# Performance work log

Measured on AMD Instinct MI355X. Metric: run time of the kernel, lower is better.

Reference implementation:

```python
import jax, jax.numpy as jnp
import numpy as np

DIM = 512
HEADS = 16
HD = DIM // HEADS            # head_dim = 32
WH, WW = 8, 8                # window_size
D0, D1 = 2, 2                # dilated_size
TWH, TWW = WH * D0, WW * D1  # total_window_size = 16,16
SCALE = HD ** -0.5


def _wpart(x, wh, ww):
    # (B,H,W,C) -> (B * H/wh * W/ww, wh, ww, C)
    B, H, W, C = x.shape
    x = x.reshape(B, H // wh, wh, W // ww, ww, C)
    return x.transpose(0, 1, 3, 2, 4, 5).reshape(-1, wh, ww, C)


def _wrev(win, wh, ww, H, W):
    # (nW*B, wh, ww, C) -> (B, H, W, C)
    C = win.shape[-1]
    B = win.shape[0] // ((H // wh) * (W // ww))
    x = win.reshape(B, H // wh, W // ww, wh, ww, C).transpose(0, 1, 3, 2, 4, 5)
    return x.reshape(B, H, W, C)


def _rope2(x):
    # 2D RoPE over a (B, WH, WW, HD) window: first half of HD rotated by row
    # position, second half by column position (axial rotary embedding).
    d = HD // 2
    inv = 1.0 / (10000.0 ** (jnp.arange(0, d, 2, dtype=jnp.float32) / d))  # (d/2,)

    def rot(xp, ang):
        x1, x2 = xp[..., 0::2], xp[..., 1::2]
        c, s = jnp.cos(ang), jnp.sin(ang)
        return jnp.stack([x1 * c - x2 * s, x1 * s + x2 * c], axis=-1).reshape(xp.shape)

    ah = (jnp.arange(WH, dtype=jnp.float32)[:, None] * inv)[:, None, :]  # (WH,1,d/2)
    aw = (jnp.arange(WW, dtype=jnp.float32)[:, None] * inv)[None, :, :]  # (1,WW,d/2)
    return jnp.concatenate([rot(x[..., :d], ah), rot(x[..., d:], aw)], axis=-1)


def _forward(x, qkv_w, qkv_b, proj_w, proj_b):
    B, H, W, C = x.shape
    # partition into total windows, then dilated regrouping
    xw = _wpart(x, TWH, TWW)                                   # (B_, 16, 16, C)
    B_ = xw.shape[0]
    xw = _wpart(xw, D0, D1)                                    # (B_*64, 2, 2, C)
    xw = xw.reshape(B_, WH * WW, D0 * D1, C)
    xw = xw.transpose(0, 2, 1, 3).reshape(B_ * D0 * D1, WH * WW, C)  # (B__, N, C)
    B__, N = xw.shape[0], xw.shape[1]

    qkv = (xw @ qkv_w.T + qkv_b).reshape(B__, N, 3, HEADS, HD).transpose(2, 0, 3, 1, 4)
    q, k, v = qkv[0], qkv[1], qkv[2]                           # (B__, HEADS, N, HD)

    q = _rope2(q.reshape(-1, WH, WW, HD)).reshape(B__, HEADS, N, HD) * SCALE
    k = _rope2(k.reshape(-1, WH, WW, HD)).reshape(B__, HEADS, N, HD)

    attn = jax.nn.softmax(jnp.einsum('bhnd,bhmd->bhnm', q, k), axis=-1)
    out = jnp.einsum('bhnm,bhmd->bhnd', attn, v)               # (B__, HEADS, N, HD)
    out = out.transpose(0, 2, 1, 3).reshape(B__, N, C)

    # undo dilated regrouping, then undo total-window partition
    out = out.reshape(B_, D0 * D1, N, C).transpose(0, 2, 1, 3).reshape(-1, D0, D1, C)
    out = _wrev(out, D0, D1, TWH, TWW)                         # (B_, 16, 16, C)
    out = _wrev(out, TWH, TWW, H, W)                           # (B, H, W, C)
    return out @ proj_w.T + proj_b


def setup_inputs() -> dict:
    key = jax.random.key(0)
    k0, k1, k2 = jax.random.split(key, 3)
    x = jax.random.normal(k0, (4, 128, 128, DIM), dtype=jnp.float32)
    qkv_w = jax.random.normal(k1, (3 * DIM, DIM), dtype=jnp.float32) * (DIM ** -0.5)
    qkv_b = jnp.zeros((3 * DIM,), dtype=jnp.float32)
    proj_w = jax.random.normal(k2, (DIM, DIM), dtype=jnp.float32) * (DIM ** -0.5)
    proj_b = jnp.zeros((DIM,), dtype=jnp.float32)
    return {"x": x, "qkv_w": qkv_w, "qkv_b": qkv_b, "proj_w": proj_w, "proj_b": proj_b}


def reference(x, qkv_w, qkv_b, proj_w, proj_b):
    return _forward(x, qkv_w, qkv_b, proj_w, proj_b)
```

## Files before the change

### kernel.cpp

```cpp
#include <hip/hip_runtime.h>
#include <hip/hip_bf16.h>
#include <stdint.h>

#define DIMC  512
#define NHEAD 16
#define HDIM  32
#define NTOK  65536
#define QKVN  1536
static constexpr float SCALE_F = 0.17677669529663687f;

typedef __attribute__((ext_vector_type(4))) float  f32x4;
typedef __attribute__((ext_vector_type(8))) __bf16 bf16x8;

__device__ __forceinline__ uint16_t f2bf(float f) {
  union { float f; uint32_t u; } v; v.f = f;
  return (uint16_t)((v.u + 0x7FFFu + ((v.u >> 16) & 1u)) >> 16);
}

__device__ __forceinline__ void gload_lds16(const void* g, void* l) {
  __builtin_amdgcn_global_load_lds((const __attribute__((address_space(1))) void*)g,
                                   (__attribute__((address_space(3))) void*)l,
                                   16, 0, 0);
}

__global__ void cvt_f32_bf16(const float* __restrict__ src,
                             uint16_t* __restrict__ dst, int n4)
{
  int i = blockIdx.x * blockDim.x + threadIdx.x;
  const int stride = gridDim.x * blockDim.x;
  for (; i < n4; i += stride) {
    const float4 v = ((const float4*)src)[i];
    ushort4 o;
    o.x = f2bf(v.x); o.y = f2bf(v.y); o.z = f2bf(v.z); o.w = f2bf(v.w);
    ((ushort4*)dst)[i] = o;
  }
}

template <bool OUT_F32>
__global__ __launch_bounds__(256, 2)
void gemm_bias_bf16(const uint16_t* __restrict__ A,
                    const uint16_t* __restrict__ B,
                    const float* __restrict__ bias,
                    void* __restrict__ Cv,
                    int M, int N, int K)
{
  __shared__ __align__(16) __bf16 As[128][64];
  __shared__ __align__(16) __bf16 Bs[128][64];

  const int tid = threadIdx.x;
  const int l  = tid & 63, w = tid >> 6;
  const int wm = w >> 1,  wn = w & 1;
  const int lm = l & 15,  lq = l >> 4;
  const long m0 = (long)blockIdx.y * 128;
  const long n0 = (long)blockIdx.x * 128;

  const int srow = tid >> 3;
  const int scol = (tid & 7) * 8;
  const uint16_t* Ag = A + (m0 + srow) * (long)K + scol;
  const uint16_t* Bg = B + (n0 + srow) * (long)K + scol;
  char* AsW = (char*)(&As[0][0]) + w * 1024;
  char* BsW = (char*)(&Bs[0][0]) + w * 1024;

  f32x4 acc[4][4] = {};

  for (int kt = 0; kt < K; kt += 64) {
#pragma unroll
    for (int c = 0; c < 4; ++c)
      gload_lds16(Ag + (size_t)c * 32 * K + kt, AsW + c * 4096);
#pragma unroll
    for (int c = 0; c < 4; ++c)
      gload_lds16(Bg + (size_t)c * 32 * K + kt, BsW + c * 4096);
    __syncthreads();

#pragma unroll
    for (int kk = 0; kk < 2; ++kk) {
      bf16x8 a[4], b[4];
#pragma unroll
      for (int i = 0; i < 4; ++i)
        a[i] = *(const bf16x8*)(&As[wm * 64 + i * 16 + lm][kk * 32 + lq * 8]);
#pragma unroll
      for (int i = 0; i < 4; ++i)
        b[i] = *(const bf16x8*)(&Bs[wn * 64 + i * 16 + lm][kk * 32 + lq * 8]);
#pragma unroll
      for (int mi = 0; mi < 4; ++mi)
#pragma unroll
        for (int ni = 0; ni < 4; ++ni)
          acc[mi][ni] = __builtin_amdgcn_mfma_f32_16x16x32_bf16(
              a[mi], b[ni], acc[mi][ni], 0, 0, 0);
    }
    __syncthreads();
  }

  float bvals[4];
#pragma unroll
  for (int ni = 0; ni < 4; ++ni)
    bvals[ni] = bias[n0 + wn * 64 + ni * 16 + lm];

#pragma unroll
  for (int mi = 0; mi < 4; ++mi)
#pragma unroll
    for (int ni = 0; ni < 4; ++ni) {
      long m = m0 + wm * 64 + mi * 16 + lq * 4;
      long n = n0 + wn * 64 + ni * 16 + lm;
#pragma unroll
      for (int r = 0; r < 4; ++r) {
        const float val = acc[mi][ni][r] + bvals[ni];
        if (OUT_F32) ((float*)Cv)[(m + r) * (long)N + n] = val;
        else         ((uint16_t*)Cv)[(m + r) * (long)N + n] = f2bf(val);
      }
    }
}

__global__ void attn_win(const uint16_t* __restrict__ QKV,
                         uint16_t* __restrict__ O)
{
  __shared__ __align__(16) __bf16 Pl[4][64][72];

  const int tid = threadIdx.x;
  const int l  = tid & 63, w = tid >> 6;
  const int lm = l & 15,  lq = l >> 4;
  const int bid = blockIdx.x;
  const int g = bid >> 2;
  const int h = (bid & 3) * 4 + w;

  const int d1 = g & 1, d0 = (g >> 1) & 1;
  const int wx = (g >> 2) & 7, wy = (g >> 5) & 7, bb = g >> 8;
  const long tbase = ((long)(bb * 128 + wy * 16 + d0) * 128) + wx * 16 + d1;

  f32x4 invs;
#pragma unroll
  for (int i = 0; i < 4; ++i)
    invs[i] = exp2f(-1.6609640474436813f * (float)((lq & 1) * 4 + i));

  const int co_q = h * HDIM;
  const int co_k = DIMC + h * HDIM;
  const int co_v = 2 * DIMC + h * HDIM;

  bf16x8 qf[4], kf[4];
#pragma unroll
  for (int f = 0; f < 4; ++f) {
    const int n  = f * 16 + lm;
    const int iy = n >> 3, ix = n & 7;
    const float pos = (lq < 2) ? (float)iy : (float)ix;
    const long t = tbase + iy * 256 + ix * 2;
    const uint16_t* qp = QKV + t * QKVN + co_q + lq * 8;
    const uint16_t* kp = QKV + t * QKVN + co_k + lq * 8;
    {
      bf16x8 raw = *(const bf16x8*)qp, o;
#pragma unroll
      for (int i = 0; i < 4; ++i) {
        float x1 = (float)raw[2 * i], x2 = (float)raw[2 * i + 1];
        float s, c; __sincosf(pos * invs[i], &s, &c);
        o[2 * i]     = (__bf16)((x1 * c - x2 * s) * SCALE_F);
        o[2 * i + 1] = (__bf16)((x1 * s + x2 * c) * SCALE_F);
      }
      qf[f] = o;
    }
    {
      bf16x8 raw = *(const bf16x8*)kp, o;
#pragma unroll
      for (int i = 0; i < 4; ++i) {
        float x1 = (float)raw[2 * i], x2 = (float)raw[2 * i + 1];
        float s, c; __sincosf(pos * invs[i], &s, &c);
        o[2 * i]     = (__bf16)(x1 * c - x2 * s);
        o[2 * i + 1] = (__bf16)(x1 * s + x2 * c);
      }
      kf[f] = o;
    }
  }

  const f32x4 fzero = {0.f, 0.f, 0.f, 0.f};
  f32x4 s[4][4];
#pragma unroll
  for (int mi = 0; mi < 4; ++mi)
#pragma unroll
    for (int ni = 0; ni < 4; ++ni)
      s[mi][ni] = __builtin_amdgcn_mfma_f32_16x16x32_bf16(qf[mi], kf[ni], fzero, 0, 0, 0);

  float rsum[4][4];
#pragma unroll
  for (int mi = 0; mi < 4; ++mi)
#pragma unroll
    for (int r = 0; r < 4; ++r) {
      float m = s[mi][0][r];
#pragma unroll
      for (int ni = 1; ni < 4; ++ni) m = fmaxf(m, s[mi][ni][r]);
      m = fmaxf(m, __shfl_xor(m, 1));
      m = fmaxf(m, __shfl_xor(m, 2));
      m = fmaxf(m, __shfl_xor(m, 4));
      m = fmaxf(m, __shfl_xor(m, 8));
      float sum = 0.f;
#pragma unroll
      for (int ni = 0; ni < 4; ++ni) {
        float p = expf(s[mi][ni][r] - m);
        s[mi][ni][r] = p;
        sum += p;
      }
      sum += __shfl_xor(sum, 1);
      sum += __shfl_xor(sum, 2);
      sum += __shfl_xor(sum, 4);
      sum += __shfl_xor(sum, 8);
      rsum[mi][r] = sum;
    }

#pragma unroll
  for (int mi = 0; mi < 4; ++mi)
#pragma unroll
    for (int ni = 0; ni < 4; ++ni)
#pragma unroll
      for (int r = 0; r < 4; ++r)
        Pl[w][mi * 16 + lq * 4 + r][ni * 16 + lm] = (__bf16)s[mi][ni][r];

  bf16x8 pa[4][2];
#pragma unroll
  for (int mi = 0; mi < 4; ++mi)
#pragma unroll
    for (int kk = 0; kk < 2; ++kk)
      pa[mi][kk] = *(const bf16x8*)(&Pl[w][mi * 16 + lm][kk * 32 + lq * 8]);

  bf16x8 vf[2][2];
#pragma unroll
  for (int kk = 0; kk < 2; ++kk)
#pragma unroll
    for (int n2 = 0; n2 < 2; ++n2) {
      const int nb = kk * 32 + lq * 8;
      const long tb2 = tbase + (long)(nb >> 3) * 256;
      const uint16_t* vp = QKV + co_v + n2 * 16 + lm;
      bf16x8 o;
#pragma unroll
      for (int i = 0; i < 8; ++i)
        o[i] = *(const __bf16*)(vp + (tb2 + 2 * i) * QKVN);
      vf[kk][n2] = o;
    }

  f32x4 oacc[4][2] = {};
#pragma unroll
  for (int kk = 0; kk < 2; ++kk)
#pragma unroll
    for (int mi = 0; mi < 4; ++mi)
#pragma unroll
      for (int n2 = 0; n2 < 2; ++n2)
        oacc[mi][n2] = __builtin_amdgcn_mfma_f32_16x16x32_bf16(
            pa[mi][kk], vf[kk][n2], oacc[mi][n2], 0, 0, 0);

#pragma unroll
  for (int mi = 0; mi < 4; ++mi)
#pragma unroll
    for (int r = 0; r < 4; ++r) {
      const int n = mi * 16 + lq * 4 + r;
      const long t = tbase + (n >> 3) * 256 + (n & 7) * 2;
      const float rinv = 1.0f / rsum[mi][r];
#pragma unroll
      for (int n2 = 0; n2 < 2; ++n2)
        O[t * DIMC + h * HDIM + n2 * 16 + lm] = f2bf(oacc[mi][n2][r] * rinv);
    }
}

extern "C" void kernel_launch(void* const* d_in, const int* in_sizes, int n_in,
                              void* d_out, int out_size, void* d_ws, size_t ws_size,
                              hipStream_t stream)
{
  const float* x      = (const float*)d_in[0];
  const float* qkv_w  = (const float*)d_in[1];
  const float* qkv_b  = (const float*)d_in[2];
  const float* proj_w = (const float*)d_in[3];
  const float* proj_b = (const float*)d_in[4];
  float* out = (float*)d_out;

  uint16_t* xb    = (uint16_t*)d_ws;
  uint16_t* qwb   = xb    + (size_t)NTOK * DIMC;
  uint16_t* pwb   = qwb   + (size_t)QKVN * DIMC;
  uint16_t* qkv   = pwb   + (size_t)DIMC * DIMC;
  uint16_t* attn  = qkv   + (size_t)NTOK * QKVN;

  cvt_f32_bf16<<<2048, 256, 0, stream>>>(x,      xb,  NTOK * DIMC / 4);
  cvt_f32_bf16<<<512,  256, 0, stream>>>(qkv_w,  qwb, QKVN * DIMC / 4);
  cvt_f32_bf16<<<256,  256, 0, stream>>>(proj_w, pwb, DIMC * DIMC / 4);

  gemm_bias_bf16<false><<<dim3(QKVN / 128, NTOK / 128), dim3(256), 0, stream>>>(
      xb, qwb, qkv_b, qkv, NTOK, QKVN, DIMC);

  attn_win<<<dim3(1024 * 4), dim3(256), 0, stream>>>(qkv, attn);

  gemm_bias_bf16<true><<<dim3(DIMC / 128, NTOK / 128), dim3(256), 0, stream>>>(
      attn, pwb, proj_b, out, NTOK, DIMC, DIMC);
}
```

Before: 317.6 us.

## Replace GEMM with 256x256 tiled, double-buffered 8-phase pipelined kernel

```diff
diff --git a/kernel.cpp b/kernel.cpp
--- a/kernel.cpp
+++ b/kernel.cpp
@@ -37,78 +37,117 @@
 }
 
 template <bool OUT_F32>
-__global__ __launch_bounds__(256, 2)
-void gemm_bias_bf16(const uint16_t* __restrict__ A,
-                    const uint16_t* __restrict__ B,
-                    const float* __restrict__ bias,
-                    void* __restrict__ Cv,
-                    int M, int N, int K)
+__global__ __launch_bounds__(512, 2)
+void gemm256_8ph(const uint16_t* __restrict__ A,
+                 const uint16_t* __restrict__ B,
+                 const float* __restrict__ bias,
+                 void* __restrict__ Cv,
+                 int M, int N, int K, int gx)
 {
-  __shared__ __align__(16) __bf16 As[128][64];
-  __shared__ __align__(16) __bf16 Bs[128][64];
+  __shared__ __align__(16) char lds[131072];
 
   const int tid = threadIdx.x;
   const int l  = tid & 63, w = tid >> 6;
-  const int wm = w >> 1,  wn = w & 1;
+  const int wm = w >> 2,  wn = w & 3;
   const int lm = l & 15,  lq = l >> 4;
-  const long m0 = (long)blockIdx.y * 128;
-  const long n0 = (long)blockIdx.x * 128;
-
-  const int srow = tid >> 3;
-  const int scol = (tid & 7) * 8;
-  const uint16_t* Ag = A + (m0 + srow) * (long)K + scol;
-  const uint16_t* Bg = B + (n0 + srow) * (long)K + scol;
-  char* AsW = (char*)(&As[0][0]) + w * 1024;
-  char* BsW = (char*)(&Bs[0][0]) + w * 1024;
-
-  f32x4 acc[4][4] = {};
-
-  for (int kt = 0; kt < K; kt += 64) {
-#pragma unroll
-    for (int c = 0; c < 4; ++c)
-      gload_lds16(Ag + (size_t)c * 32 * K + kt, AsW + c * 4096);
-#pragma unroll
-    for (int c = 0; c < 4; ++c)
-      gload_lds16(Bg + (size_t)c * 32 * K + kt, BsW + c * 4096);
-    __syncthreads();
-
-#pragma unroll
-    for (int kk = 0; kk < 2; ++kk) {
-      bf16x8 a[4], b[4];
-#pragma unroll
-      for (int i = 0; i < 4; ++i)
-        a[i] = *(const bf16x8*)(&As[wm * 64 + i * 16 + lm][kk * 32 + lq * 8]);
-#pragma unroll
-      for (int i = 0; i < 4; ++i)
-        b[i] = *(const bf16x8*)(&Bs[wn * 64 + i * 16 + lm][kk * 32 + lq * 8]);
-#pragma unroll
-      for (int mi = 0; mi < 4; ++mi)
-#pragma unroll
-        for (int ni = 0; ni < 4; ++ni)
-          acc[mi][ni] = __builtin_amdgcn_mfma_f32_16x16x32_bf16(
-              a[mi], b[ni], acc[mi][ni], 0, 0, 0);
-    }
-    __syncthreads();
-  }
-
-  float bvals[4];
-#pragma unroll
-  for (int ni = 0; ni < 4; ++ni)
-    bvals[ni] = bias[n0 + wn * 64 + ni * 16 + lm];
-
-#pragma unroll
-  for (int mi = 0; mi < 4; ++mi)
-#pragma unroll
-    for (int ni = 0; ni < 4; ++ni) {
-      long m = m0 + wm * 64 + mi * 16 + lq * 4;
-      long n = n0 + wn * 64 + ni * 16 + lm;
-#pragma unroll
-      for (int r = 0; r < 4; ++r) {
-        const float val = acc[mi][ni][r] + bvals[ni];
-        if (OUT_F32) ((float*)Cv)[(m + r) * (long)N + n] = val;
-        else         ((uint16_t*)Cv)[(m + r) * (long)N + n] = f2bf(val);
-      }
-    }
+
+  const int nwg = gridDim.x;
+  const int qq = nwg >> 3, rr = nwg & 7;
+  const int xcd = blockIdx.x & 7, loc = blockIdx.x >> 3;
+  const int sw = (xcd < rr ? xcd * (qq + 1) : rr * (qq + 1) + (xcd - rr) * qq) + loc;
+  const long m0 = (long)(sw / gx) * 256;
+  const long n0 = (long)(sw % gx) * 256;
+
+  const int srow  = tid >> 3;
+  const int scolb = (((tid & 7) ^ (srow & 7)) << 4);
+  const uint16_t* Ags = A + (m0 + srow) * (long)K + (scolb >> 1);
+  const uint16_t* Bgs = B + (n0 + srow) * (long)K + (scolb >> 1);
+  char* ldsW = lds + (w << 10);
+
+  auto STAGE = [&](const uint16_t* Gs, int regionOff, int half, int kt) {
+    const uint16_t* s0 = Gs + (size_t)(half * 128) * K + kt;
+    gload_lds16(s0,                 ldsW + regionOff);
+    gload_lds16(s0 + (size_t)64 * K, ldsW + regionOff + 8192);
+  };
+
+  const int colx0 = ((lq ^ (lm & 7)) << 4);
+  const int aoff0 = (wm * 64 + lm) * 128 + colx0;
+  const int aoff1 = (wm * 64 + lm) * 128 + (colx0 ^ 64);
+  const int boff0 = (wn * 32 + lm) * 128 + colx0;
+  const int boff1 = (wn * 32 + lm) * 128 + (colx0 ^ 64);
+
+  f32x4 acc[2][2][4][2] = {};
+
+#define PHASE(SLOT, QM, QN, STG, VM)                                          \
+  {                                                                           \
+    const char* Ab = lds + (SLOT) * 65536 + (QM) * 16384;                     \
+    const char* Bb = lds + (SLOT) * 65536 + 32768 + (QN) * 16384;             \
+    bf16x8 af0[4], af1[4], bq0[2], bq1[2];                                    \
+    _Pragma("unroll") for (int i = 0; i < 4; ++i) {                           \
+      af0[i] = *(const bf16x8*)(Ab + aoff0 + i * 2048);                       \
+      af1[i] = *(const bf16x8*)(Ab + aoff1 + i * 2048);                       \
+    }                                                                         \
+    _Pragma("unroll") for (int j = 0; j < 2; ++j) {                           \
+      bq0[j] = *(const bf16x8*)(Bb + boff0 + j * 2048);                       \
+      bq1[j] = *(const bf16x8*)(Bb + boff1 + j * 2048);                       \
+    }                                                                         \
+    STG;                                                                      \
+    __builtin_amdgcn_s_barrier();                                             \
+    __builtin_amdgcn_s_setprio(1);                                            \
+    _Pragma("unroll") for (int i = 0; i < 4; ++i)                             \
+      _Pragma("unroll") for (int j = 0; j < 2; ++j) {                         \
+        acc[QM][QN][i][j] = __builtin_amdgcn_mfma_f32_16x16x32_bf16(          \
+            af0[i], bq0[j], acc[QM][QN][i][j], 0, 0, 0);                      \
+        acc[QM][QN][i][j] = __builtin_amdgcn_mfma_f32_16x16x32_bf16(          \
+            af1[i], bq1[j], acc[QM][QN][i][j], 0, 0, 0);                      \
+      }                                                                       \
+    __builtin_amdgcn_s_setprio(0);                                            \
+    if (VM) { asm volatile("s_waitcnt vmcnt(4)" ::: "memory"); }              \
+    __builtin_amdgcn_s_barrier();                                             \
+  }
+
+  STAGE(Ags, 0,             0, 0);
+  STAGE(Bgs, 32768,         0, 0);
+  STAGE(Ags, 16384,         1, 0);
+  STAGE(Bgs, 49152,         1, 0);
+  STAGE(Ags, 65536,         0, 64);
+  STAGE(Bgs, 65536 + 32768, 0, 64);
+  asm volatile("s_waitcnt vmcnt(4)" ::: "memory");
+  __builtin_amdgcn_s_barrier();
+
+  for (int t2 = 0; t2 < K / 64; t2 += 2) {
+    const int k1 = (t2 + 1) * 64;
+    int k2 = (t2 + 2) * 64; if (k2 >= K) k2 = 0;
+    int k3 = (t2 + 3) * 64; if (k3 >= K) k3 = 0;
+    PHASE(0, 0, 0, STAGE(Ags, 65536 + 16384, 1, k1), 0)
+    PHASE(0, 0, 1, STAGE(Bgs, 65536 + 49152, 1, k1), 0)
+    PHASE(0, 1, 0, STAGE(Ags, 0,             0, k2), 0)
+    PHASE(0, 1, 1, STAGE(Bgs, 32768,         0, k2), 1)
+    PHASE(1, 0, 0, STAGE(Ags, 16384,         1, k2), 0)
+    PHASE(1, 0, 1, STAGE(Bgs, 49152,         1, k2), 0)
+    PHASE(1, 1, 0, STAGE(Ags, 65536,         0, k3), 0)
+    PHASE(1, 1, 1, STAGE(Bgs, 65536 + 32768, 0, k3), 1)
+  }
+#undef PHASE
+
+#pragma unroll
+  for (int qm = 0; qm < 2; ++qm)
+#pragma unroll
+  for (int qn = 0; qn < 2; ++qn)
+#pragma unroll
+  for (int i = 0; i < 4; ++i)
+#pragma unroll
+  for (int j = 0; j < 2; ++j) {
+    const long m = m0 + qm * 128 + wm * 64 + i * 16 + lq * 4;
+    const long n = n0 + qn * 128 + wn * 32 + j * 16 + lm;
+    const float bv = bias[n];
+#pragma unroll
+    for (int r = 0; r < 4; ++r) {
+      const float val = acc[qm][qn][i][j][r] + bv;
+      if (OUT_F32) ((float*)Cv)[(m + r) * (long)N + n] = val;
+      else         ((uint16_t*)Cv)[(m + r) * (long)N + n] = f2bf(val);
+    }
+  }
 }
 
 __global__ void attn_win(const uint16_t* __restrict__ QKV,
@@ -277,11 +316,11 @@
   cvt_f32_bf16<<<512,  256, 0, stream>>>(qkv_w,  qwb, QKVN * DIMC / 4);
   cvt_f32_bf16<<<256,  256, 0, stream>>>(proj_w, pwb, DIMC * DIMC / 4);
 
-  gemm_bias_bf16<false><<<dim3(QKVN / 128, NTOK / 128), dim3(256), 0, stream>>>(
-      xb, qwb, qkv_b, qkv, NTOK, QKVN, DIMC);
+  gemm256_8ph<false><<<dim3((NTOK / 256) * (QKVN / 256)), dim3(512), 0, stream>>>(
+      xb, qwb, qkv_b, qkv, NTOK, QKVN, DIMC, QKVN / 256);
 
   attn_win<<<dim3(1024 * 4), dim3(256), 0, stream>>>(qkv, attn);
 
-  gemm_bias_bf16<true><<<dim3(DIMC / 128, NTOK / 128), dim3(256), 0, stream>>>(
-      attn, pwb, proj_b, out, NTOK, DIMC, DIMC);
-}
+  gemm256_8ph<true><<<dim3((NTOK / 256) * (DIMC / 256)), dim3(512), 0, stream>>>(
+      attn, pwb, proj_b, out, NTOK, DIMC, DIMC, DIMC / 256);
+}
```

New measurement: 304.2 us. 4.2% less time.

## Fuse x fp32-to-bf16 conversion into QKV GEMM with swizzled LDS and XCD remap

Applied to the files above, without the earlier changes.

```diff
diff --git a/kernel.cpp b/kernel.cpp
--- a/kernel.cpp
+++ b/kernel.cpp
@@ -36,13 +36,13 @@
   }
 }
 
-template <bool OUT_F32>
-__global__ __launch_bounds__(256, 2)
-void gemm_bias_bf16(const uint16_t* __restrict__ A,
-                    const uint16_t* __restrict__ B,
-                    const float* __restrict__ bias,
-                    void* __restrict__ Cv,
-                    int M, int N, int K)
+template <bool A_F32, bool OUT_F32>
+__global__ __launch_bounds__(256, 3)
+void gemm128_tlp(const void* __restrict__ Av,
+                 const uint16_t* __restrict__ B,
+                 const float* __restrict__ bias,
+                 void* __restrict__ Cv,
+                 int M, int N, int K, int gx)
 {
   __shared__ __align__(16) __bf16 As[128][64];
   __shared__ __align__(16) __bf16 Bs[128][64];
@@ -51,36 +51,86 @@
   const int l  = tid & 63, w = tid >> 6;
   const int wm = w >> 1,  wn = w & 1;
   const int lm = l & 15,  lq = l >> 4;
-  const long m0 = (long)blockIdx.y * 128;
-  const long n0 = (long)blockIdx.x * 128;
-
-  const int srow = tid >> 3;
-  const int scol = (tid & 7) * 8;
-  const uint16_t* Ag = A + (m0 + srow) * (long)K + scol;
-  const uint16_t* Bg = B + (n0 + srow) * (long)K + scol;
-  char* AsW = (char*)(&As[0][0]) + w * 1024;
-  char* BsW = (char*)(&Bs[0][0]) + w * 1024;
+
+  const int nwg = gridDim.x;
+  const int qq = nwg >> 3, rr = nwg & 7;
+  const int xcd = blockIdx.x & 7, loc = blockIdx.x >> 3;
+  const int sw = (xcd < rr ? xcd * (qq + 1) : rr * (qq + 1) + (xcd - rr) * qq) + loc;
+  const long m0 = (long)(sw / gx) * 128;
+  const long n0 = (long)(sw % gx) * 128;
+
+  char* AsC = (char*)&As[0][0];
+  char* BsC = (char*)&Bs[0][0];
+
+  const int dr  = w * 8 + (l >> 3);
+  const int su  = (l & 7) ^ ((l >> 3) & 7);
+  const uint16_t* Bg = B + (n0 + dr) * (long)K + su * 8;
+  const uint16_t* Ag16 = A_F32 ? nullptr
+                       : (const uint16_t*)Av + (m0 + dr) * (long)K + su * 8;
+
+  const int ar   = tid >> 3;
+  const int ac8  = (tid & 7) * 8;
+  const int aswz = (tid & 7) ^ ((tid >> 3) & 7);
+  const float* Agf = A_F32 ? (const float*)Av + (m0 + ar) * (long)K + ac8 : nullptr;
+
+  f32x4 alo[4], ahi[4];
+  if (A_F32) {
+#pragma unroll
+    for (int j = 0; j < 4; ++j) {
+      alo[j] = *(const f32x4*)(Agf + (size_t)j * 32 * K);
+      ahi[j] = *(const f32x4*)(Agf + (size_t)j * 32 * K + 4);
+    }
+  }
 
   f32x4 acc[4][4] = {};
 
   for (int kt = 0; kt < K; kt += 64) {
+    __syncthreads();
+
+    if (A_F32) {
+#pragma unroll
+      for (int j = 0; j < 4; ++j) {
+        bf16x8 v;
+#pragma unroll
+        for (int q = 0; q < 4; ++q) {
+          v[q]     = (__bf16)alo[j][q];
+          v[q + 4] = (__bf16)ahi[j][q];
+        }
+        *(bf16x8*)(AsC + (j * 32 + ar) * 128 + aswz * 16) = v;
+      }
+    } else {
+#pragma unroll
+      for (int c = 0; c < 4; ++c)
+        gload_lds16(Ag16 + (size_t)c * 32 * K + kt, AsC + w * 1024 + c * 4096);
+    }
 #pragma unroll
     for (int c = 0; c < 4; ++c)
-      gload_lds16(Ag + (size_t)c * 32 * K + kt, AsW + c * 4096);
-#pragma unroll
-    for (int c = 0; c < 4; ++c)
-      gload_lds16(Bg + (size_t)c * 32 * K + kt, BsW + c * 4096);
+      gload_lds16(Bg + (size_t)c * 32 * K + kt, BsC + w * 1024 + c * 4096);
+
     __syncthreads();
+
+    if (A_F32) {
+      const int kt2 = (kt + 64 < K) ? kt + 64 : 0;
+#pragma unroll
+      for (int j = 0; j < 4; ++j) {
+        alo[j] = *(const f32x4*)(Agf + (size_t)j * 32 * K + kt2);
+        ahi[j] = *(const f32x4*)(Agf + (size_t)j * 32 * K + kt2 + 4);
+      }
+    }
 
 #pragma unroll
     for (int kk = 0; kk < 2; ++kk) {
       bf16x8 a[4], b[4];
 #pragma unroll
-      for (int i = 0; i < 4; ++i)
-        a[i] = *(const bf16x8*)(&As[wm * 64 + i * 16 + lm][kk * 32 + lq * 8]);
-#pragma unroll
-      for (int i = 0; i < 4; ++i)
-        b[i] = *(const bf16x8*)(&Bs[wn * 64 + i * 16 + lm][kk * 32 + lq * 8]);
+      for (int i = 0; i < 4; ++i) {
+        const int ra = wm * 64 + i * 16 + lm;
+        a[i] = *(const bf16x8*)(AsC + ra * 128 + (((kk * 4 + lq) ^ (lm & 7)) << 4));
+      }
+#pragma unroll
+      for (int i = 0; i < 4; ++i) {
+        const int rb = wn * 64 + i * 16 + lm;
+        b[i] = *(const bf16x8*)(BsC + rb * 128 + (((kk * 4 + lq) ^ (lm & 7)) << 4));
+      }
 #pragma unroll
       for (int mi = 0; mi < 4; ++mi)
 #pragma unroll
@@ -88,7 +138,6 @@
           acc[mi][ni] = __builtin_amdgcn_mfma_f32_16x16x32_bf16(
               a[mi], b[ni], acc[mi][ni], 0, 0, 0);
     }
-    __syncthreads();
   }
 
   float bvals[4];
@@ -100,8 +149,8 @@
   for (int mi = 0; mi < 4; ++mi)
 #pragma unroll
     for (int ni = 0; ni < 4; ++ni) {
-      long m = m0 + wm * 64 + mi * 16 + lq * 4;
-      long n = n0 + wn * 64 + ni * 16 + lm;
+      const long m = m0 + wm * 64 + mi * 16 + lq * 4;
+      const long n = n0 + wn * 64 + ni * 16 + lm;
 #pragma unroll
       for (int r = 0; r < 4; ++r) {
         const float val = acc[mi][ni][r] + bvals[ni];
@@ -267,21 +316,19 @@
   const float* proj_b = (const float*)d_in[4];
   float* out = (float*)d_out;
 
-  uint16_t* xb    = (uint16_t*)d_ws;
-  uint16_t* qwb   = xb    + (size_t)NTOK * DIMC;
-  uint16_t* pwb   = qwb   + (size_t)QKVN * DIMC;
-  uint16_t* qkv   = pwb   + (size_t)DIMC * DIMC;
-  uint16_t* attn  = qkv   + (size_t)NTOK * QKVN;
-
-  cvt_f32_bf16<<<2048, 256, 0, stream>>>(x,      xb,  NTOK * DIMC / 4);
-  cvt_f32_bf16<<<512,  256, 0, stream>>>(qkv_w,  qwb, QKVN * DIMC / 4);
-  cvt_f32_bf16<<<256,  256, 0, stream>>>(proj_w, pwb, DIMC * DIMC / 4);
-
-  gemm_bias_bf16<false><<<dim3(QKVN / 128, NTOK / 128), dim3(256), 0, stream>>>(
-      xb, qwb, qkv_b, qkv, NTOK, QKVN, DIMC);
+  uint16_t* qwb  = (uint16_t*)d_ws;
+  uint16_t* pwb  = qwb + (size_t)QKVN * DIMC;
+  uint16_t* qkv  = pwb + (size_t)DIMC * DIMC;
+  uint16_t* attn = qkv + (size_t)NTOK * QKVN;
+
+  cvt_f32_bf16<<<512, 256, 0, stream>>>(qkv_w,  qwb, QKVN * DIMC / 4);
+  cvt_f32_bf16<<<256, 256, 0, stream>>>(proj_w, pwb, DIMC * DIMC / 4);
+
+  gemm128_tlp<true, false><<<dim3((NTOK / 128) * (QKVN / 128)), dim3(256), 0, stream>>>(
+      x, qwb, qkv_b, qkv, NTOK, QKVN, DIMC, QKVN / 128);
 
   attn_win<<<dim3(1024 * 4), dim3(256), 0, stream>>>(qkv, attn);
 
-  gemm_bias_bf16<true><<<dim3(DIMC / 128, NTOK / 128), dim3(256), 0, stream>>>(
-      attn, pwb, proj_b, out, NTOK, DIMC, DIMC);
-}
+  gemm128_tlp<false, true><<<dim3((NTOK / 128) * (DIMC / 128)), dim3(256), 0, stream>>>(
+      attn, pwb, proj_b, out, NTOK, DIMC, DIMC, DIMC / 128);
+}
```

Result: faster. 301.8 us (median of 2 runs) (-5.0%).
